# Optimization experiments

Hardware: AMD Instinct MI355X
Metric: run time of the kernel (lower is better)

The kernel has to match this reference:

```python
import jax, jax.numpy as jnp
import numpy as np

B, C, H, W = 8, 256, 128, 128
QK = 64

def setup_inputs() -> dict:
    key = jax.random.key(0)
    ks = jax.random.split(key, 8)
    s = 0.02
    return {
        "x": jax.random.normal(ks[0], (B, C, H, W), dtype=jnp.float32),
        "wq": jax.random.normal(ks[1], (QK, C), dtype=jnp.float32) * s,
        "bq": jax.random.normal(ks[2], (QK,), dtype=jnp.float32) * s,
        "wk": jax.random.normal(ks[3], (QK, C), dtype=jnp.float32) * s,
        "bk": jax.random.normal(ks[4], (QK,), dtype=jnp.float32) * s,
        "wv": jax.random.normal(ks[5], (C, C), dtype=jnp.float32) * s,
        "bv": jax.random.normal(ks[6], (C,), dtype=jnp.float32) * s,
        "gamma": jax.random.normal(ks[7], (1,), dtype=jnp.float32) * 0.1,
    }

def reference(x, wq, bq, wk, bk, wv, bv, gamma):
    # 1x1 convs == per-pixel linear projections over channels
    Q = jnp.einsum('bchw,oc->bohw', x, wq) + bq[None, :, None, None]  # (b,qk,h,w)
    K = jnp.einsum('bchw,oc->bohw', x, wk) + bk[None, :, None, None]  # (b,qk,h,w)
    V = jnp.einsum('bchw,oc->bohw', x, wv) + bv[None, :, None, None]  # (b,c,h,w)
    # row attention: for each (b,h) row, scores over width pairs
    scores = jnp.einsum('bchw,bchv->bhwv', Q, K)          # (b,h,w_q,w_k)
    attn = jax.nn.softmax(scores, axis=-1)                # softmax over keys (dim=2 after bmm)
    out = jnp.einsum('bchv,bhwv->bchw', V, attn)          # (b,c,h,w)
    return gamma[0] * out + x
```

## Files before the change

### kernel.cpp

```cpp
#include <hip/hip_runtime.h>
#include <hip/hip_bf16.h>


typedef short bf16x8 __attribute__((ext_vector_type(8)));
typedef float f32x4 __attribute__((ext_vector_type(4)));
using u32 = unsigned int;
using u16 = unsigned short;

#define XT_OFF   0
#define XT_SB    528
#define SA_OFF   67584
#define SB_OFF   85056
#define QT_OFF   67584
#define KT_OFF   86016
#define QK_SB    144
#define PL_OFF   67584
#define PL_SB    272
#define WP_OFF   104448
#define VL_OFF   141312
#define VL_SB    272
#define SMP_OFF  141312
#define BIAS_OFF 158720
#define LDS_TOTAL 160256

#define WS_WQK   0
#define WS_WV    73728

__device__ __forceinline__ u16 bfbits(float f) {
    __hip_bfloat16 h = __float2bfloat16(f);
    u16 u; __builtin_memcpy(&u, &h, 2); return u;
}
__device__ __forceinline__ u32 packbf2(float a, float b) {
    return (u32)bfbits(a) | ((u32)bfbits(b) << 16);
}
__device__ __forceinline__ float bf2f(u16 u) {
    union { u32 i; float f; } v; v.i = ((u32)u) << 16; return v.f;
}

__device__ __forceinline__ void gl2lds16(const char* g, const char* l) {
    __builtin_amdgcn_global_load_lds(
        (const __attribute__((address_space(1))) void*)(unsigned long long)g,
        (__attribute__((address_space(3))) void*)(u32)(unsigned long long)l,
        16, 0, 0);
}
__device__ __forceinline__ void stage18k(const char* g, const char* lds, int w, int l) {
    gl2lds16(g + w * 1024 + l * 16, lds + w * 1024);
    if (l < 8) gl2lds16(g + 16384 + w * 128 + l * 16, lds + 16384 + w * 128);
}
__device__ __forceinline__ void stage36k(const char* g, const char* lds, int w, int l) {
    gl2lds16(g + w * 1024 + l * 16,         lds + w * 1024);
    gl2lds16(g + 16384 + w * 1024 + l * 16, lds + 16384 + w * 1024);
    if (l < 16) gl2lds16(g + 32768 + w * 256 + l * 16, lds + 32768 + w * 256);
}

__device__ __forceinline__ void hard_barrier() {
    __builtin_amdgcn_sched_barrier(0);
    asm volatile("s_barrier" ::: "memory");
    __builtin_amdgcn_sched_barrier(0);
}
__device__ __forceinline__ void lgkm_barrier() {
    __builtin_amdgcn_sched_barrier(0);
    asm volatile("s_waitcnt lgkmcnt(0)\n\ts_barrier" ::: "memory");
    __builtin_amdgcn_sched_barrier(0);
}

__global__ void prep_weights(const float* __restrict__ wq, const float* __restrict__ wk,
                             const float* __restrict__ wv, u32* __restrict__ ws) {
    int i = blockIdx.x * 256 + threadIdx.x;
    if (i >= 55296) return;
    u32 v = 0;
    if (i < 18432) {
        int c = i / 2304, rem = i % 2304;
        int row = rem / 36, iw = rem % 36;
        int kc = c >> 1;
        const float* m = (c & 1) ? wk : wq;
        if (iw < 32) {
            int col = kc * 64 + iw * 2;
            v = packbf2(m[row * 256 + col], m[row * 256 + col + 1]);
        }
    } else {
        int j = i - 18432;
        int c = j / 2304, rem = j % 2304;
        int row = rem / 36, iw = rem % 36;
        int mc = c >> 2, kc = c & 3;
        if (iw < 32) {
            int col = kc * 64 + iw * 2;
            v = packbf2(wv[(mc * 64 + row) * 256 + col], wv[(mc * 64 + row) * 256 + col + 1]);
        }
    }
    ws[i] = v;
}

__global__ __launch_bounds__(1024, 1) void rowattn_mfma(
    const float* __restrict__ x,
    const float* __restrict__ bq,
    const float* __restrict__ bk,
    const float* __restrict__ bv,
    const float* __restrict__ gamma,
    const char* __restrict__ wsp,
    float* __restrict__ out)
{
    __shared__ __align__(16) char smem[LDS_TOTAL];
    const int t  = threadIdx.x;
    const int bh = blockIdx.x;
    const int b  = bh >> 7;
    const int h  = bh & 127;
    const int l  = t & 63;
    const int a  = l & 15;
    const int q  = l >> 4;
    const int wid = __builtin_amdgcn_readfirstlane(t >> 6);
    const int mi = wid >> 2;
    const int nj = wid & 3;
    const int w0 = nj * 32;

    const char* wqk_g = wsp + WS_WQK;
    const char* wv_g  = wsp + WS_WV;
    const float g = gamma[0];

    stage18k(wqk_g,         smem + WP_OFF,         wid, l);
    stage18k(wqk_g + 18432, smem + WP_OFF + 18432, wid, l);

    float* biasl = (float*)(smem + BIAS_OFF);
    if (t < 384) {
        float v;
        if (t < 64) v = bq[t];
        else if (t < 128) v = bk[t - 64];
        else v = bv[t - 128];
        biasl[t] = v;
    }

    const int cl = t >> 5;
    const int w4 = (t & 31) * 4;
    const float* xb = x + ((b * 256 + cl) * 128 + h) * 128 + w4;
    float4 xr[8];
#pragma unroll
    for (int p = 0; p < 8; ++p) xr[p] = *(const float4*)(xb + (p * 32) * 16384);

    const int wrd = t >> 3;
    const int c4  = (t & 7) * 4;
#define SCW(c, w) ((c) * 136 + ((c) >> 3) * 8 + (w))
    {
        float* s0 = (float*)(smem + SA_OFF);
        *(float4*)&s0[SCW(cl, w4)] = xr[0];
    }
    lgkm_barrier();
#pragma unroll
    for (int p = 0; p < 8; ++p) {
        float* sp = (float*)(smem + ((p & 1) ? SB_OFF : SA_OFF));
        if (p < 7) {
            float* sn = (float*)(smem + ((p & 1) ? SA_OFF : SB_OFF));
            *(float4*)&sn[SCW(cl, w4)] = xr[p + 1];
        }
        const float* sr = sp + SCW(c4, wrd);
        float s0 = sr[0], s1 = sr[136], s2 = sr[2 * 136], s3 = sr[3 * 136];
        uint2 pk; pk.x = packbf2(s0, s1); pk.y = packbf2(s2, s3);
        *(uint2*)(smem + XT_OFF + wrd * XT_SB + (p * 32 + c4) * 2) = pk;
        if (p < 7) lgkm_barrier();
    }
#undef SCW
    __syncthreads();

    {
        f32x4 accQ[2], accK[2];
#pragma unroll
        for (int nt = 0; nt < 2; ++nt) {
            f32x4 cq, ck;
#pragma unroll
            for (int r = 0; r < 4; ++r) {
                cq[r] = biasl[mi * 16 + q * 4 + r];
                ck[r] = biasl[64 + mi * 16 + q * 4 + r];
            }
            accQ[nt] = cq; accK[nt] = ck;
        }
#pragma unroll
        for (int kc = 0; kc < 4; ++kc) {
            if (kc == 2) {
                asm volatile("s_waitcnt vmcnt(2)" ::: "memory");
                hard_barrier();
            }
            if (kc == 3) __syncthreads();
            const char* wqp = smem + WP_OFF + (kc & 1) * 18432;
            const char* wkp = wqp + 9216;
#pragma unroll
            for (int ks = 0; ks < 2; ++ks) {
                bf16x8 aq = *(const bf16x8*)(wqp + (mi * 16 + a) * 144 + ks * 64 + q * 16);
                bf16x8 ak = *(const bf16x8*)(wkp + (mi * 16 + a) * 144 + ks * 64 + q * 16);
#pragma unroll
                for (int nt = 0; nt < 2; ++nt) {
                    bf16x8 bx = *(const bf16x8*)(smem + XT_OFF + (w0 + nt * 16 + a) * XT_SB + (kc * 64 + ks * 32) * 2 + q * 16);
                    accQ[nt] = __builtin_amdgcn_mfma_f32_16x16x32_bf16(aq, bx, accQ[nt], 0, 0, 0);
                    accK[nt] = __builtin_amdgcn_mfma_f32_16x16x32_bf16(ak, bx, accK[nt], 0, 0, 0);
                }
            }
            if (kc == 0) { hard_barrier(); stage18k(wqk_g + 2 * 18432, smem + WP_OFF,         wid, l); }
            if (kc == 1) { hard_barrier(); stage18k(wqk_g + 3 * 18432, smem + WP_OFF + 18432, wid, l); }
        }
#pragma unroll
        for (int nt = 0; nt < 2; ++nt) {
            const int wrow = w0 + nt * 16 + a;
            uint2 pq; pq.x = packbf2(accQ[nt][0], accQ[nt][1]); pq.y = packbf2(accQ[nt][2], accQ[nt][3]);
            *(uint2*)(smem + QT_OFF + wrow * QK_SB + (mi * 16 + q * 4) * 2) = pq;
            uint2 pk; pk.x = packbf2(accK[nt][0], accK[nt][1]); pk.y = packbf2(accK[nt][2], accK[nt][3]);
            *(uint2*)(smem + KT_OFF + wrow * QK_SB + (mi * 16 + q * 4) * 2) = pk;
        }
    }
    __syncthreads();

    stage36k(wv_g, smem + WP_OFF, wid, l);
    f32x4 st[2][2];
#pragma unroll
    for (int mt2 = 0; mt2 < 2; ++mt2)
#pragma unroll
        for (int nt = 0; nt < 2; ++nt) st[mt2][nt] = (f32x4){0.f, 0.f, 0.f, 0.f};
#pragma unroll
    for (int ks = 0; ks < 2; ++ks) {
        bf16x8 bq0 = *(const bf16x8*)(smem + QT_OFF + (w0 + a) * QK_SB + ks * 64 + q * 16);
        bf16x8 bq1 = *(const bf16x8*)(smem + QT_OFF + (w0 + 16 + a) * QK_SB + ks * 64 + q * 16);
        bf16x8 ak0 = *(const bf16x8*)(smem + KT_OFF + (mi * 32 + a) * QK_SB + ks * 64 + q * 16);
        bf16x8 ak1 = *(const bf16x8*)(smem + KT_OFF + (mi * 32 + 16 + a) * QK_SB + ks * 64 + q * 16);
        st[0][0] = __builtin_amdgcn_mfma_f32_16x16x32_bf16(ak0, bq0, st[0][0], 0, 0, 0);
        st[0][1] = __builtin_amdgcn_mfma_f32_16x16x32_bf16(ak0, bq1, st[0][1], 0, 0, 0);
        st[1][0] = __builtin_amdgcn_mfma_f32_16x16x32_bf16(ak1, bq0, st[1][0], 0, 0, 0);
        st[1][1] = __builtin_amdgcn_mfma_f32_16x16x32_bf16(ak1, bq1, st[1][1], 0, 0, 0);
    }
    {
        float pmax[2], psum[2];
#pragma unroll
        for (int nt = 0; nt < 2; ++nt) {
            float mx = -3.0e38f;
#pragma unroll
            for (int mt2 = 0; mt2 < 2; ++mt2)
#pragma unroll
                for (int r = 0; r < 4; ++r) mx = fmaxf(mx, st[mt2][nt][r]);
            mx = fmaxf(mx, __shfl_xor(mx, 16, 64));
            mx = fmaxf(mx, __shfl_xor(mx, 32, 64));
            float s = 0.f;
#pragma unroll
            for (int mt2 = 0; mt2 < 2; ++mt2)
#pragma unroll
                for (int r = 0; r < 4; ++r) {
                    float e = __expf(st[mt2][nt][r] - mx); st[mt2][nt][r] = e; s += e;
                }
            s += __shfl_xor(s, 16, 64);
            s += __shfl_xor(s, 32, 64);
            pmax[nt] = mx; psum[nt] = s;
        }
        float2* smp = (float2*)(smem + SMP_OFF);
        if (q == 0) {
#pragma unroll
            for (int nt = 0; nt < 2; ++nt)
                smp[(w0 + nt * 16 + a) * 4 + mi] = make_float2(pmax[nt], psum[nt]);
        }
        lgkm_barrier();
        float f[2];
#pragma unroll
        for (int nt = 0; nt < 2; ++nt) {
            const int wq = w0 + nt * 16 + a;
            float2 p0 = smp[wq * 4 + 0], p1 = smp[wq * 4 + 1];
            float2 p2 = smp[wq * 4 + 2], p3 = smp[wq * 4 + 3];
            float m = fmaxf(fmaxf(p0.x, p1.x), fmaxf(p2.x, p3.x));
            float s = p0.y * __expf(p0.x - m) + p1.y * __expf(p1.x - m)
                    + p2.y * __expf(p2.x - m) + p3.y * __expf(p3.x - m);
            f[nt] = __expf(pmax[nt] - m) / s;
        }
#pragma unroll
        for (int nt = 0; nt < 2; ++nt) {
            const int wq = w0 + nt * 16 + a;
#pragma unroll
            for (int mt2 = 0; mt2 < 2; ++mt2) {
                uint2 pp;
                pp.x = packbf2(st[mt2][nt][0] * f[nt], st[mt2][nt][1] * f[nt]);
                pp.y = packbf2(st[mt2][nt][2] * f[nt], st[mt2][nt][3] * f[nt]);
                *(uint2*)(smem + PL_OFF + wq * PL_SB + (mi * 32 + mt2 * 16 + q * 4) * 2) = pp;
            }
        }
    }

#pragma unroll 1
    for (int mc = 0; mc < 4; ++mc) {
        __syncthreads();
        f32x4 accV[2];
        {
            f32x4 cv;
#pragma unroll
            for (int r = 0; r < 4; ++r) cv[r] = biasl[128 + mc * 64 + mi * 16 + q * 4 + r];
            accV[0] = cv; accV[1] = cv;
        }
#pragma unroll
        for (int kc = 0; kc < 4; ++kc) {
            const char* wvp = smem + WP_OFF + kc * 9216;
#pragma unroll
            for (int ks = 0; ks < 2; ++ks) {
                bf16x8 av = *(const bf16x8*)(wvp + (mi * 16 + a) * 144 + ks * 64 + q * 16);
#pragma unroll
                for (int nt = 0; nt < 2; ++nt) {
                    bf16x8 bx = *(const bf16x8*)(smem + XT_OFF + (w0 + nt * 16 + a) * XT_SB + (kc * 64 + ks * 32) * 2 + q * 16);
                    accV[nt] = __builtin_amdgcn_mfma_f32_16x16x32_bf16(av, bx, accV[nt], 0, 0, 0);
                }
            }
        }
#pragma unroll
        for (int nt = 0; nt < 2; ++nt)
#pragma unroll
            for (int r = 0; r < 4; ++r)
                *(u16*)(smem + VL_OFF + (mi * 16 + q * 4 + r) * VL_SB + (w0 + nt * 16 + a) * 2) = bfbits(accV[nt][r]);
        __syncthreads();
        if (mc < 3) stage36k(wv_g + (mc + 1) * 36864, smem + WP_OFF, wid, l);
        f32x4 accO[2];
        accO[0] = (f32x4){0.f, 0.f, 0.f, 0.f};
        accO[1] = (f32x4){0.f, 0.f, 0.f, 0.f};
#pragma unroll
        for (int ks = 0; ks < 4; ++ks) {
            bf16x8 av = *(const bf16x8*)(smem + VL_OFF + (mi * 16 + a) * VL_SB + ks * 64 + q * 16);
#pragma unroll
            for (int nt = 0; nt < 2; ++nt) {
                bf16x8 bp = *(const bf16x8*)(smem + PL_OFF + (w0 + nt * 16 + a) * PL_SB + ks * 64 + q * 16);
                accO[nt] = __builtin_amdgcn_mfma_f32_16x16x32_bf16(av, bp, accO[nt], 0, 0, 0);
            }
        }
#pragma unroll
        for (int r = 0; r < 4; ++r) {
            const int c = mc * 64 + mi * 16 + q * 4 + r;
            float* orow = out + ((b * 256 + c) * 128 + h) * 128;
#pragma unroll
            for (int nt = 0; nt < 2; ++nt) {
                const int w = w0 + nt * 16 + a;
                u16 xv = *(const u16*)(smem + XT_OFF + w * XT_SB + c * 2);
                orow[w] = g * accO[nt][r] + bf2f(xv);
            }
        }
    }
}

extern "C" void kernel_launch(void* const* d_in, const int* in_sizes, int n_in,
                              void* d_out, int out_size, void* d_ws, size_t ws_size,
                              hipStream_t stream) {
    const float* x     = (const float*)d_in[0];
    const float* wq    = (const float*)d_in[1];
    const float* bq    = (const float*)d_in[2];
    const float* wk    = (const float*)d_in[3];
    const float* bk    = (const float*)d_in[4];
    const float* wv    = (const float*)d_in[5];
    const float* bv    = (const float*)d_in[6];
    const float* gamma = (const float*)d_in[7];
    float* out = (float*)d_out;

    hipLaunchKernelGGL(prep_weights, dim3(216), dim3(256), 0, stream, wq, wk, wv, (u32*)d_ws);
    hipLaunchKernelGGL(rowattn_mfma, dim3(1024), dim3(1024), 0, stream,
                       x, bq, bk, bv, gamma, (const char*)d_ws, out);
}
```

Measured before the change: 295.5 us.

## Process four rows per block with register-prefetched x and weights

Each block now handles four consecutive h rows instead of one, launching 256 blocks instead of 1024, so that with 256 CUs every block is resident at once. The next row's x is loaded into registers while the current row's V projection and output run. Weight staging switches from direct global-to-LDS loads to register loads that are written to LDS after barriers, which lets them overlap with MFMA work. The x transpose no longer goes through an fp32 LDS staging buffer. Each thread writes its bf16 x values straight into the transposed layout with strided scalar loads. The risks are fewer blocks to hide latency, more register pressure from the 32-value x prefetch, and less coalesced x reads.

```diff
diff --git a/kernel.cpp b/kernel.cpp
--- a/kernel.cpp
+++ b/kernel.cpp
@@ -9,8 +9,6 @@
 
 #define XT_OFF   0
 #define XT_SB    528
-#define SA_OFF   67584
-#define SB_OFF   85056
 #define QT_OFF   67584
 #define KT_OFF   86016
 #define QK_SB    144
@@ -37,27 +35,6 @@
     union { u32 i; float f; } v; v.i = ((u32)u) << 16; return v.f;
 }
 
-__device__ __forceinline__ void gl2lds16(const char* g, const char* l) {
-    __builtin_amdgcn_global_load_lds(
-        (const __attribute__((address_space(1))) void*)(unsigned long long)g,
-        (__attribute__((address_space(3))) void*)(u32)(unsigned long long)l,
-        16, 0, 0);
-}
-__device__ __forceinline__ void stage18k(const char* g, const char* lds, int w, int l) {
-    gl2lds16(g + w * 1024 + l * 16, lds + w * 1024);
-    if (l < 8) gl2lds16(g + 16384 + w * 128 + l * 16, lds + 16384 + w * 128);
-}
-__device__ __forceinline__ void stage36k(const char* g, const char* lds, int w, int l) {
-    gl2lds16(g + w * 1024 + l * 16,         lds + w * 1024);
-    gl2lds16(g + 16384 + w * 1024 + l * 16, lds + 16384 + w * 1024);
-    if (l < 16) gl2lds16(g + 32768 + w * 256 + l * 16, lds + 32768 + w * 256);
-}
-
-__device__ __forceinline__ void hard_barrier() {
-    __builtin_amdgcn_sched_barrier(0);
-    asm volatile("s_barrier" ::: "memory");
-    __builtin_amdgcn_sched_barrier(0);
-}
 __device__ __forceinline__ void lgkm_barrier() {
     __builtin_amdgcn_sched_barrier(0);
     asm volatile("s_waitcnt lgkmcnt(0)\n\ts_barrier" ::: "memory");
@@ -102,9 +79,6 @@
 {
     __shared__ __align__(16) char smem[LDS_TOTAL];
     const int t  = threadIdx.x;
-    const int bh = blockIdx.x;
-    const int b  = bh >> 7;
-    const int h  = bh & 127;
     const int l  = t & 63;
     const int a  = l & 15;
     const int q  = l >> 4;
@@ -113,12 +87,38 @@
     const int nj = wid & 3;
     const int w0 = nj * 32;
 
+    const int blk = blockIdx.x;
+    const int b   = blk >> 5;
+    const int h0  = (blk << 2) & 127;
+
     const char* wqk_g = wsp + WS_WQK;
     const char* wv_g  = wsp + WS_WV;
-    const float g = gamma[0];
-
-    stage18k(wqk_g,         smem + WP_OFF,         wid, l);
-    stage18k(wqk_g + 18432, smem + WP_OFF + 18432, wid, l);
+
+    const int xw  = ((wid & 8) << 3) + l;
+    const int xcb = (wid & 7) * 4;
+    const float* xbase = x + (size_t)(b * 256 + xcb) * 16384 + xw;
+    float xv[32];
+    {
+        const float* xp = xbase + h0 * 128;
+#pragma unroll
+        for (int p = 0; p < 8; ++p)
+#pragma unroll
+            for (int j = 0; j < 4; ++j)
+                xv[p * 4 + j] = xp[(p * 32 + j) * 16384];
+    }
+
+    {
+        uint4 p0a = *(const uint4*)(wqk_g + t * 16);
+        uint4 p1a = *(const uint4*)(wqk_g + 18432 + t * 16);
+        *(uint4*)(smem + WP_OFF + t * 16) = p0a;
+        *(uint4*)(smem + WP_OFF + 18432 + t * 16) = p1a;
+        if (t < 128) {
+            uint4 p0b = *(const uint4*)(wqk_g + 16384 + t * 16);
+            uint4 p1b = *(const uint4*)(wqk_g + 18432 + 16384 + t * 16);
+            *(uint4*)(smem + WP_OFF + 16384 + t * 16) = p0b;
+            *(uint4*)(smem + WP_OFF + 18432 + 16384 + t * 16) = p1b;
+        }
+    }
 
     float* biasl = (float*)(smem + BIAS_OFF);
     if (t < 384) {
@@ -128,57 +128,45 @@
         else v = bv[t - 128];
         biasl[t] = v;
     }
-
-    const int cl = t >> 5;
-    const int w4 = (t & 31) * 4;
-    const float* xb = x + ((b * 256 + cl) * 128 + h) * 128 + w4;
-    float4 xr[8];
-#pragma unroll
-    for (int p = 0; p < 8; ++p) xr[p] = *(const float4*)(xb + (p * 32) * 16384);
-
-    const int wrd = t >> 3;
-    const int c4  = (t & 7) * 4;
-#define SCW(c, w) ((c) * 136 + ((c) >> 3) * 8 + (w))
-    {
-        float* s0 = (float*)(smem + SA_OFF);
-        *(float4*)&s0[SCW(cl, w4)] = xr[0];
-    }
-    lgkm_barrier();
-#pragma unroll
-    for (int p = 0; p < 8; ++p) {
-        float* sp = (float*)(smem + ((p & 1) ? SB_OFF : SA_OFF));
-        if (p < 7) {
-            float* sn = (float*)(smem + ((p & 1) ? SA_OFF : SB_OFF));
-            *(float4*)&sn[SCW(cl, w4)] = xr[p + 1];
-        }
-        const float* sr = sp + SCW(c4, wrd);
-        float s0 = sr[0], s1 = sr[136], s2 = sr[2 * 136], s3 = sr[3 * 136];
-        uint2 pk; pk.x = packbf2(s0, s1); pk.y = packbf2(s2, s3);
-        *(uint2*)(smem + XT_OFF + wrd * XT_SB + (p * 32 + c4) * 2) = pk;
-        if (p < 7) lgkm_barrier();
-    }
-#undef SCW
-    __syncthreads();
-
-    {
+    const float g = gamma[0];
+
+    uint4 wva, wvb, wvc;
+
+#pragma unroll 1
+    for (int r = 0; r < 4; ++r) {
+        const int h = h0 + r;
+        if (r) lgkm_barrier();
+
+#pragma unroll
+        for (int p = 0; p < 8; ++p) {
+            uint2 pk;
+            pk.x = packbf2(xv[p * 4 + 0], xv[p * 4 + 1]);
+            pk.y = packbf2(xv[p * 4 + 2], xv[p * 4 + 3]);
+            *(uint2*)(smem + XT_OFF + xw * XT_SB + (xcb + p * 32) * 2) = pk;
+        }
+
+        uint4 p2a = *(const uint4*)(wqk_g + 2 * 18432 + t * 16);
+        uint4 p3a = *(const uint4*)(wqk_g + 3 * 18432 + t * 16);
+        uint4 p2b, p3b;
+        if (t < 128) {
+            p2b = *(const uint4*)(wqk_g + 2 * 18432 + 16384 + t * 16);
+            p3b = *(const uint4*)(wqk_g + 3 * 18432 + 16384 + t * 16);
+        }
+
+        lgkm_barrier();
+
         f32x4 accQ[2], accK[2];
-#pragma unroll
-        for (int nt = 0; nt < 2; ++nt) {
+        {
             f32x4 cq, ck;
 #pragma unroll
-            for (int r = 0; r < 4; ++r) {
-                cq[r] = biasl[mi * 16 + q * 4 + r];
-                ck[r] = biasl[64 + mi * 16 + q * 4 + r];
-            }
-            accQ[nt] = cq; accK[nt] = ck;
+            for (int rr = 0; rr < 4; ++rr) {
+                cq[rr] = biasl[mi * 16 + q * 4 + rr];
+                ck[rr] = biasl[64 + mi * 16 + q * 4 + rr];
+            }
+            accQ[0] = cq; accQ[1] = cq; accK[0] = ck; accK[1] = ck;
         }
 #pragma unroll
         for (int kc = 0; kc < 4; ++kc) {
-            if (kc == 2) {
-                asm volatile("s_waitcnt vmcnt(2)" ::: "memory");
-                hard_barrier();
-            }
-            if (kc == 3) __syncthreads();
             const char* wqp = smem + WP_OFF + (kc & 1) * 18432;
             const char* wkp = wqp + 9216;
 #pragma unroll
@@ -192,8 +180,20 @@
                     accK[nt] = __builtin_amdgcn_mfma_f32_16x16x32_bf16(ak, bx, accK[nt], 0, 0, 0);
                 }
             }
-            if (kc == 0) { hard_barrier(); stage18k(wqk_g + 2 * 18432, smem + WP_OFF,         wid, l); }
-            if (kc == 1) { hard_barrier(); stage18k(wqk_g + 3 * 18432, smem + WP_OFF + 18432, wid, l); }
+            if (kc == 0) {
+                lgkm_barrier();
+                *(uint4*)(smem + WP_OFF + t * 16) = p2a;
+                if (t < 128) *(uint4*)(smem + WP_OFF + 16384 + t * 16) = p2b;
+            }
+            if (kc == 1) {
+                lgkm_barrier();
+                *(uint4*)(smem + WP_OFF + 18432 + t * 16) = p3a;
+                if (t < 128) *(uint4*)(smem + WP_OFF + 18432 + 16384 + t * 16) = p3b;
+                wva = *(const uint4*)(wv_g + t * 32);
+                wvb = *(const uint4*)(wv_g + t * 32 + 16);
+                if (t < 256) wvc = *(const uint4*)(wv_g + 32768 + t * 16);
+            }
+            if (kc == 2) lgkm_barrier();
         }
 #pragma unroll
         for (int nt = 0; nt < 2; ++nt) {
@@ -203,130 +203,165 @@
             uint2 pk; pk.x = packbf2(accK[nt][0], accK[nt][1]); pk.y = packbf2(accK[nt][2], accK[nt][3]);
             *(uint2*)(smem + KT_OFF + wrow * QK_SB + (mi * 16 + q * 4) * 2) = pk;
         }
-    }
-    __syncthreads();
-
-    stage36k(wv_g, smem + WP_OFF, wid, l);
-    f32x4 st[2][2];
-#pragma unroll
-    for (int mt2 = 0; mt2 < 2; ++mt2)
-#pragma unroll
-        for (int nt = 0; nt < 2; ++nt) st[mt2][nt] = (f32x4){0.f, 0.f, 0.f, 0.f};
-#pragma unroll
-    for (int ks = 0; ks < 2; ++ks) {
-        bf16x8 bq0 = *(const bf16x8*)(smem + QT_OFF + (w0 + a) * QK_SB + ks * 64 + q * 16);
-        bf16x8 bq1 = *(const bf16x8*)(smem + QT_OFF + (w0 + 16 + a) * QK_SB + ks * 64 + q * 16);
-        bf16x8 ak0 = *(const bf16x8*)(smem + KT_OFF + (mi * 32 + a) * QK_SB + ks * 64 + q * 16);
-        bf16x8 ak1 = *(const bf16x8*)(smem + KT_OFF + (mi * 32 + 16 + a) * QK_SB + ks * 64 + q * 16);
-        st[0][0] = __builtin_amdgcn_mfma_f32_16x16x32_bf16(ak0, bq0, st[0][0], 0, 0, 0);
-        st[0][1] = __builtin_amdgcn_mfma_f32_16x16x32_bf16(ak0, bq1, st[0][1], 0, 0, 0);
-        st[1][0] = __builtin_amdgcn_mfma_f32_16x16x32_bf16(ak1, bq0, st[1][0], 0, 0, 0);
-        st[1][1] = __builtin_amdgcn_mfma_f32_16x16x32_bf16(ak1, bq1, st[1][1], 0, 0, 0);
-    }
-    {
-        float pmax[2], psum[2];
-#pragma unroll
-        for (int nt = 0; nt < 2; ++nt) {
-            float mx = -3.0e38f;
-#pragma unroll
-            for (int mt2 = 0; mt2 < 2; ++mt2)
-#pragma unroll
-                for (int r = 0; r < 4; ++r) mx = fmaxf(mx, st[mt2][nt][r]);
-            mx = fmaxf(mx, __shfl_xor(mx, 16, 64));
-            mx = fmaxf(mx, __shfl_xor(mx, 32, 64));
-            float s = 0.f;
-#pragma unroll
-            for (int mt2 = 0; mt2 < 2; ++mt2)
-#pragma unroll
-                for (int r = 0; r < 4; ++r) {
-                    float e = __expf(st[mt2][nt][r] - mx); st[mt2][nt][r] = e; s += e;
-                }
-            s += __shfl_xor(s, 16, 64);
-            s += __shfl_xor(s, 32, 64);
-            pmax[nt] = mx; psum[nt] = s;
-        }
-        float2* smp = (float2*)(smem + SMP_OFF);
-        if (q == 0) {
+        lgkm_barrier();
+        *(uint4*)(smem + WP_OFF + t * 32) = wva;
+        *(uint4*)(smem + WP_OFF + t * 32 + 16) = wvb;
+        if (t < 256) *(uint4*)(smem + WP_OFF + 32768 + t * 16) = wvc;
+
+        f32x4 st[2][2];
+#pragma unroll
+        for (int mt2 = 0; mt2 < 2; ++mt2)
+#pragma unroll
+            for (int nt = 0; nt < 2; ++nt) st[mt2][nt] = (f32x4){0.f, 0.f, 0.f, 0.f};
+#pragma unroll
+        for (int ks = 0; ks < 2; ++ks) {
+            bf16x8 bq0 = *(const bf16x8*)(smem + QT_OFF + (w0 + a) * QK_SB + ks * 64 + q * 16);
+            bf16x8 bq1 = *(const bf16x8*)(smem + QT_OFF + (w0 + 16 + a) * QK_SB + ks * 64 + q * 16);
+            bf16x8 ak0 = *(const bf16x8*)(smem + KT_OFF + (mi * 32 + a) * QK_SB + ks * 64 + q * 16);
+            bf16x8 ak1 = *(const bf16x8*)(smem + KT_OFF + (mi * 32 + 16 + a) * QK_SB + ks * 64 + q * 16);
+            st[0][0] = __builtin_amdgcn_mfma_f32_16x16x32_bf16(ak0, bq0, st[0][0], 0, 0, 0);
+            st[0][1] = __builtin_amdgcn_mfma_f32_16x16x32_bf16(ak0, bq1, st[0][1], 0, 0, 0);
+            st[1][0] = __builtin_amdgcn_mfma_f32_16x16x32_bf16(ak1, bq0, st[1][0], 0, 0, 0);
+            st[1][1] = __builtin_amdgcn_mfma_f32_16x16x32_bf16(ak1, bq1, st[1][1], 0, 0, 0);
+        }
+        {
+            float pmax[2], psum[2];
+#pragma unroll
+            for (int nt = 0; nt < 2; ++nt) {
+                float mx = -3.0e38f;
+#pragma unroll
+                for (int mt2 = 0; mt2 < 2; ++mt2)
+#pragma unroll
+                    for (int rr = 0; rr < 4; ++rr) mx = fmaxf(mx, st[mt2][nt][rr]);
+                mx = fmaxf(mx, __shfl_xor(mx, 16, 64));
+                mx = fmaxf(mx, __shfl_xor(mx, 32, 64));
+                float s = 0.f;
+#pragma unroll
+                for (int mt2 = 0; mt2 < 2; ++mt2)
+#pragma unroll
+                    for (int rr = 0; rr < 4; ++rr) {
+                        float e = __expf(st[mt2][nt][rr] - mx); st[mt2][nt][rr] = e; s += e;
+                    }
+                s += __shfl_xor(s, 16, 64);
+                s += __shfl_xor(s, 32, 64);
+                pmax[nt] = mx; psum[nt] = s;
+            }
+            float2* smp = (float2*)(smem + SMP_OFF);
+            if (q == 0) {
+#pragma unroll
+                for (int nt = 0; nt < 2; ++nt)
+                    smp[(w0 + nt * 16 + a) * 4 + mi] = make_float2(pmax[nt], psum[nt]);
+            }
+            lgkm_barrier();
+            float f[2];
+#pragma unroll
+            for (int nt = 0; nt < 2; ++nt) {
+                const int wq = w0 + nt * 16 + a;
+                float2 pp0 = smp[wq * 4 + 0], pp1 = smp[wq * 4 + 1];
+                float2 pp2 = smp[wq * 4 + 2], pp3 = smp[wq * 4 + 3];
+                float m = fmaxf(fmaxf(pp0.x, pp1.x), fmaxf(pp2.x, pp3.x));
+                float s = pp0.y * __expf(pp0.x - m) + pp1.y * __expf(pp1.x - m)
+                        + pp2.y * __expf(pp2.x - m) + pp3.y * __expf(pp3.x - m);
+                f[nt] = __expf(pmax[nt] - m) / s;
+            }
+#pragma unroll
+            for (int nt = 0; nt < 2; ++nt) {
+                const int wq = w0 + nt * 16 + a;
+#pragma unroll
+                for (int mt2 = 0; mt2 < 2; ++mt2) {
+                    uint2 pp;
+                    pp.x = packbf2(st[mt2][nt][0] * f[nt], st[mt2][nt][1] * f[nt]);
+                    pp.y = packbf2(st[mt2][nt][2] * f[nt], st[mt2][nt][3] * f[nt]);
+                    *(uint2*)(smem + PL_OFF + wq * PL_SB + (mi * 32 + mt2 * 16 + q * 4) * 2) = pp;
+                }
+            }
+        }
+
+#pragma unroll 1
+        for (int mc = 0; mc < 4; ++mc) {
+            lgkm_barrier();
+            if (mc == 0 && r < 3) {
+                const float* xn = xbase + (h + 1) * 128;
+#pragma unroll
+                for (int p = 0; p < 8; ++p)
+#pragma unroll
+                    for (int j = 0; j < 4; ++j)
+                        xv[p * 4 + j] = xn[(p * 32 + j) * 16384];
+            }
+            if (mc < 3) {
+                wva = *(const uint4*)(wv_g + (mc + 1) * 36864 + t * 32);
+                wvb = *(const uint4*)(wv_g + (mc + 1) * 36864 + t * 32 + 16);
+                if (t < 256) wvc = *(const uint4*)(wv_g + (mc + 1) * 36864 + 32768 + t * 16);
+            }
+            uint4 n0a, n0b, n1a, n1b;
+            if (mc == 3 && r < 3) {
+                n0a = *(const uint4*)(wqk_g + t * 16);
+                n1a = *(const uint4*)(wqk_g + 18432 + t * 16);
+                if (t < 128) {
+                    n0b = *(const uint4*)(wqk_g + 16384 + t * 16);
+                    n1b = *(const uint4*)(wqk_g + 18432 + 16384 + t * 16);
+                }
+            }
+            f32x4 accV[2];
+            {
+                f32x4 cv;
+#pragma unroll
+                for (int rr = 0; rr < 4; ++rr) cv[rr] = biasl[128 + mc * 64 + mi * 16 + q * 4 + rr];
+                accV[0] = cv; accV[1] = cv;
+            }
+#pragma unroll
+            for (int kc = 0; kc < 4; ++kc) {
+                const char* wvp = smem + WP_OFF + kc * 9216;
+#pragma unroll
+                for (int ks = 0; ks < 2; ++ks) {
+                    bf16x8 av = *(const bf16x8*)(wvp + (mi * 16 + a) * 144 + ks * 64 + q * 16);
+#pragma unroll
+                    for (int nt = 0; nt < 2; ++nt) {
+                        bf16x8 bx = *(const bf16x8*)(smem + XT_OFF + (w0 + nt * 16 + a) * XT_SB + (kc * 64 + ks * 32) * 2 + q * 16);
+                        accV[nt] = __builtin_amdgcn_mfma_f32_16x16x32_bf16(av, bx, accV[nt], 0, 0, 0);
+                    }
+                }
+            }
 #pragma unroll
             for (int nt = 0; nt < 2; ++nt)
-                smp[(w0 + nt * 16 + a) * 4 + mi] = make_float2(pmax[nt], psum[nt]);
-        }
-        lgkm_barrier();
-        float f[2];
-#pragma unroll
-        for (int nt = 0; nt < 2; ++nt) {
-            const int wq = w0 + nt * 16 + a;
-            float2 p0 = smp[wq * 4 + 0], p1 = smp[wq * 4 + 1];
-            float2 p2 = smp[wq * 4 + 2], p3 = smp[wq * 4 + 3];
-            float m = fmaxf(fmaxf(p0.x, p1.x), fmaxf(p2.x, p3.x));
-            float s = p0.y * __expf(p0.x - m) + p1.y * __expf(p1.x - m)
-                    + p2.y * __expf(p2.x - m) + p3.y * __expf(p3.x - m);
-            f[nt] = __expf(pmax[nt] - m) / s;
-        }
-#pragma unroll
-        for (int nt = 0; nt < 2; ++nt) {
-            const int wq = w0 + nt * 16 + a;
-#pragma unroll
-            for (int mt2 = 0; mt2 < 2; ++mt2) {
-                uint2 pp;
-                pp.x = packbf2(st[mt2][nt][0] * f[nt], st[mt2][nt][1] * f[nt]);
-                pp.y = packbf2(st[mt2][nt][2] * f[nt], st[mt2][nt][3] * f[nt]);
-                *(uint2*)(smem + PL_OFF + wq * PL_SB + (mi * 32 + mt2 * 16 + q * 4) * 2) = pp;
-            }
-        }
-    }
-
-#pragma unroll 1
-    for (int mc = 0; mc < 4; ++mc) {
-        __syncthreads();
-        f32x4 accV[2];
-        {
-            f32x4 cv;
-#pragma unroll
-            for (int r = 0; r < 4; ++r) cv[r] = biasl[128 + mc * 64 + mi * 16 + q * 4 + r];
-            accV[0] = cv; accV[1] = cv;
-        }
-#pragma unroll
-        for (int kc = 0; kc < 4; ++kc) {
-            const char* wvp = smem + WP_OFF + kc * 9216;
-#pragma unroll
-            for (int ks = 0; ks < 2; ++ks) {
-                bf16x8 av = *(const bf16x8*)(wvp + (mi * 16 + a) * 144 + ks * 64 + q * 16);
+#pragma unroll
+                for (int rr = 0; rr < 4; ++rr)
+                    *(u16*)(smem + VL_OFF + (mi * 16 + q * 4 + rr) * VL_SB + (w0 + nt * 16 + a) * 2) = bfbits(accV[nt][rr]);
+            lgkm_barrier();
+            if (mc < 3) {
+                *(uint4*)(smem + WP_OFF + t * 32) = wva;
+                *(uint4*)(smem + WP_OFF + t * 32 + 16) = wvb;
+                if (t < 256) *(uint4*)(smem + WP_OFF + 32768 + t * 16) = wvc;
+            } else if (r < 3) {
+                *(uint4*)(smem + WP_OFF + t * 16) = n0a;
+                *(uint4*)(smem + WP_OFF + 18432 + t * 16) = n1a;
+                if (t < 128) {
+                    *(uint4*)(smem + WP_OFF + 16384 + t * 16) = n0b;
+                    *(uint4*)(smem + WP_OFF + 18432 + 16384 + t * 16) = n1b;
+                }
+            }
+            f32x4 accO[2];
+            accO[0] = (f32x4){0.f, 0.f, 0.f, 0.f};
+            accO[1] = (f32x4){0.f, 0.f, 0.f, 0.f};
+#pragma unroll
+            for (int ks = 0; ks < 4; ++ks) {
+                bf16x8 av = *(const bf16x8*)(smem + VL_OFF + (mi * 16 + a) * VL_SB + ks * 64 + q * 16);
 #pragma unroll
                 for (int nt = 0; nt < 2; ++nt) {
-                    bf16x8 bx = *(const bf16x8*)(smem + XT_OFF + (w0 + nt * 16 + a) * XT_SB + (kc * 64 + ks * 32) * 2 + q * 16);
-                    accV[nt] = __builtin_amdgcn_mfma_f32_16x16x32_bf16(av, bx, accV[nt], 0, 0, 0);
-                }
-            }
-        }
-#pragma unroll
-        for (int nt = 0; nt < 2; ++nt)
-#pragma unroll
-            for (int r = 0; r < 4; ++r)
-                *(u16*)(smem + VL_OFF + (mi * 16 + q * 4 + r) * VL_SB + (w0 + nt * 16 + a) * 2) = bfbits(accV[nt][r]);
-        __syncthreads();
-        if (mc < 3) stage36k(wv_g + (mc + 1) * 36864, smem + WP_OFF, wid, l);
-        f32x4 accO[2];
-        accO[0] = (f32x4){0.f, 0.f, 0.f, 0.f};
-        accO[1] = (f32x4){0.f, 0.f, 0.f, 0.f};
-#pragma unroll
-        for (int ks = 0; ks < 4; ++ks) {
-            bf16x8 av = *(const bf16x8*)(smem + VL_OFF + (mi * 16 + a) * VL_SB + ks * 64 + q * 16);
-#pragma unroll
-            for (int nt = 0; nt < 2; ++nt) {
-                bf16x8 bp = *(const bf16x8*)(smem + PL_OFF + (w0 + nt * 16 + a) * PL_SB + ks * 64 + q * 16);
-                accO[nt] = __builtin_amdgcn_mfma_f32_16x16x32_bf16(av, bp, accO[nt], 0, 0, 0);
-            }
-        }
-#pragma unroll
-        for (int r = 0; r < 4; ++r) {
-            const int c = mc * 64 + mi * 16 + q * 4 + r;
-            float* orow = out + ((b * 256 + c) * 128 + h) * 128;
-#pragma unroll
-            for (int nt = 0; nt < 2; ++nt) {
-                const int w = w0 + nt * 16 + a;
-                u16 xv = *(const u16*)(smem + XT_OFF + w * XT_SB + c * 2);
-                orow[w] = g * accO[nt][r] + bf2f(xv);
+                    bf16x8 bp = *(const bf16x8*)(smem + PL_OFF + (w0 + nt * 16 + a) * PL_SB + ks * 64 + q * 16);
+                    accO[nt] = __builtin_amdgcn_mfma_f32_16x16x32_bf16(av, bp, accO[nt], 0, 0, 0);
+                }
+            }
+#pragma unroll
+            for (int rr = 0; rr < 4; ++rr) {
+                const int c = mc * 64 + mi * 16 + q * 4 + rr;
+                float* orow = out + ((b * 256 + c) * 128 + h) * 128;
+#pragma unroll
+                for (int nt = 0; nt < 2; ++nt) {
+                    const int w = w0 + nt * 16 + a;
+                    u16 xvr = *(const u16*)(smem + XT_OFF + w * XT_SB + c * 2);
+                    orow[w] = g * accO[nt][rr] + bf2f(xvr);
+                }
             }
         }
     }
@@ -346,6 +381,6 @@
     float* out = (float*)d_out;
 
     hipLaunchKernelGGL(prep_weights, dim3(216), dim3(256), 0, stream, wq, wk, wv, (u32*)d_ws);
-    hipLaunchKernelGGL(rowattn_mfma, dim3(1024), dim3(1024), 0, stream,
+    hipLaunchKernelGGL(rowattn_mfma, dim3(256), dim3(1024), 0, stream,
                        x, bq, bk, bv, gamma, (const char*)d_ws, out);
 }
```

After: 376.4 us. 27.4% more time.
